# Optimization experiments

Measured on AMD Instinct MI355X. Metric: run time of the kernel, lower is better.

Reference implementation:

```python
import jax, jax.numpy as jnp
import numpy as np

N, E, IN_DIM, HID, OUT = 50000, 600000, 128, 256, 128

def setup_inputs() -> dict:
    key = jax.random.key(0)
    k1, k2, k3, k4, k5, k6, k7 = jax.random.split(key, 7)
    h = jax.random.normal(k1, (N, IN_DIM), dtype=jnp.float32)
    src = jax.random.randint(k2, (E,), 0, N)
    dst = jax.random.randint(k3, (E,), 0, N)
    s1 = 1.0 / np.sqrt(2 * IN_DIM)
    s2 = 1.0 / np.sqrt(HID)
    W1 = jax.random.uniform(k4, (2 * IN_DIM, HID), minval=-s1, maxval=s1, dtype=jnp.float32)
    b1 = jax.random.uniform(k5, (HID,), minval=-s1, maxval=s1, dtype=jnp.float32)
    W2 = jax.random.uniform(k6, (HID, OUT), minval=-s2, maxval=s2, dtype=jnp.float32)
    b2 = jax.random.uniform(k7, (OUT,), minval=-s2, maxval=s2, dtype=jnp.float32)
    return {"h": h, "src": src, "dst": dst, "W1": W1, "b1": b1, "W2": W2, "b2": b2}

def reference(h, src, dst, W1, b1, W2, b2):
    n = h.shape[0]
    # copy_u + mean: gather src features, segment-sum at dst, divide by in-degree
    msg_sum = jax.ops.segment_sum(h[src], dst, num_segments=n)          # [N, D]
    deg = jax.ops.segment_sum(jnp.ones((src.shape[0],), h.dtype), dst, num_segments=n)
    h_neigh = msg_sum / jnp.maximum(deg, 1.0)[:, None]                  # zero-deg nodes -> 0
    h_total = jnp.concatenate([h, h_neigh], axis=1)                     # [N, 2D]
    out = (h_total @ W1 + b1) @ W2 + b2                                 # 2-layer MLP (no inner activation)
    return jax.nn.relu(out)
```

## Files before the change

kernel.cpp:

```cpp
#include <hip/hip_runtime.h>

#define N_NODES 50000
#define E_EDGES 600000
#define IN_DIM  128
#define HID     256
#define OUT_DIM 128
#define CAP     64

#define NB_FILL 2344
#define NB_HCVT 6250
#define NB_WCVT 384
#define NB_PREP (NB_FILL + NB_HCVT + NB_WCVT)
#define NB_MLP  782

typedef __bf16 bf16x8 __attribute__((ext_vector_type(8)));
typedef float  f32x16 __attribute__((ext_vector_type(16)));
typedef unsigned short ushort8 __attribute__((ext_vector_type(8)));

__device__ __forceinline__ unsigned short f2bf(float f) {
    union { float f; unsigned int i; } v; v.f = f;
    unsigned int b = v.i;
    b += 0x7fffu + ((b >> 16) & 1u);
    return (unsigned short)(b >> 16);
}
__device__ __forceinline__ float bf2f(unsigned short u) {
    union { unsigned int i; float f; } v; v.i = ((unsigned int)u) << 16; return v.f;
}

__global__ void __launch_bounds__(256)
sage_prep(const int* __restrict__ src, const int* __restrict__ dst,
          int* __restrict__ counts, char* __restrict__ outb,
          const float* __restrict__ h, unsigned short* __restrict__ ht,
          const float* __restrict__ W1, const float* __restrict__ W2,
          unsigned short* __restrict__ w1sw, unsigned short* __restrict__ w2sw) {
    int i = blockIdx.x;
    int q = i >> 2, r = i & 3;
    int job, id;
    if (r == 1) { job = 0; id = q; }
    else {
        int oid = 3 * q + (r == 0 ? 0 : r - 1);
        if (oid < NB_HCVT)           { job = 1; id = oid; }
        else if (oid < NB_HCVT + NB_WCVT) { job = 2; id = oid - NB_HCVT; }
        else                         { job = 0; id = 2245 + (oid - (NB_HCVT + NB_WCVT)); }
    }

    if (job == 0) {
        int e = id * 256 + threadIdx.x;
        if (e < E_EDGES) {
            int d = dst[e];
            int slot = atomicAdd(counts + d, 1);
            if (slot < CAP)
                *((int*)(outb + (size_t)d * 512 + 256) + slot) = src[e];
        }
    } else if (job == 1) {
        int idx = id * 256 + threadIdx.x;
        if (idx < N_NODES * 32) {
            int n = idx >> 5, g = idx & 31;
            const float4 v = *(const float4*)(h + (size_t)n * IN_DIM + g * 4);
            ushort4 o;
            o.x = f2bf(v.x); o.y = f2bf(v.y); o.z = f2bf(v.z); o.w = f2bf(v.w);
            *(ushort4*)(ht + (size_t)n * 128 + g * 4) = o;
        }
    } else {
        int i1 = id * 256 + threadIdx.x;
        if (i1 < 65536) {
            int j = i1 & 7, n = (i1 >> 3) & 255, g = (i1 >> 11) & 1, ks = (i1 >> 12) & 3, c = i1 >> 14;
            int k = c * 64 + ks * 16 + g * 8 + j;
            w1sw[i1] = f2bf(W1[(size_t)k * HID + n]);
        } else {
            int i2 = i1 - 65536;
            int j = i2 & 7, n = (i2 >> 3) & 127, g = (i2 >> 10) & 1, ks = (i2 >> 11) & 7, c = (i2 >> 14) & 1;
            int k = c * 128 + ks * 16 + g * 8 + j;
            w2sw[i2] = f2bf(W2[(size_t)k * OUT_DIM + n]);
        }
    }
}

__global__ void __launch_bounds__(256)
sage_fused(const int* __restrict__ counts,
           const unsigned short* __restrict__ ht,
           const unsigned short* __restrict__ w1sw,
           const unsigned short* __restrict__ w2sw,
           const float* __restrict__ b1,
           const float* __restrict__ b2,
           float* out) {
    __shared__ unsigned short wbuf[16384];
    __shared__ unsigned short hid_s[64][264];

    const int t = threadIdx.x;
    const int nw = t >> 6;
    const int lane = t & 63;
    const int lr = lane & 31;
    const int lg = lane >> 5;
    const int base = blockIdx.x * 64;
    const int row0 = min(base + lr,      N_NODES - 1);
    const int row1 = min(base + 32 + lr, N_NODES - 1);

    {
        const bf16x8* gsrc = (const bf16x8*)(w1sw);
        #pragma unroll
        for (int i2 = 0; i2 < 8; ++i2) {
            int off16 = i2 * 256 + t;
            *(bf16x8*)(wbuf + off16 * 8) = gsrc[off16];
        }
    }

    {
        int node = base + (t >> 2);
        int l4 = t & 3;
        if (node < N_NODES) {
            int dg = counts[node];
            int entries = min(dg, CAP);
            const int* bk = (const int*)((const char*)out + (size_t)node * 512 + 256);
            float acc[32];
            #pragma unroll
            for (int j = 0; j < 32; ++j) acc[j] = 0.f;
            int e = 0;
            for (; e + 4 <= entries; e += 4) {
                const int4 sx = *(const int4*)(bk + e);
                const ushort8* p0 = (const ushort8*)(ht + (size_t)sx.x * 128 + l4 * 32);
                const ushort8* p1 = (const ushort8*)(ht + (size_t)sx.y * 128 + l4 * 32);
                const ushort8* p2 = (const ushort8*)(ht + (size_t)sx.z * 128 + l4 * 32);
                const ushort8* p3 = (const ushort8*)(ht + (size_t)sx.w * 128 + l4 * 32);
                ushort8 v00 = p0[0], v01 = p0[1], v02 = p0[2], v03 = p0[3];
                ushort8 v10 = p1[0], v11 = p1[1], v12 = p1[2], v13 = p1[3];
                ushort8 v20 = p2[0], v21 = p2[1], v22 = p2[2], v23 = p2[3];
                ushort8 v30 = p3[0], v31 = p3[1], v32 = p3[2], v33 = p3[3];
                #pragma unroll
                for (int j = 0; j < 8; ++j) {
                    acc[j]      += bf2f(v00[j]) + bf2f(v10[j]) + bf2f(v20[j]) + bf2f(v30[j]);
                    acc[8 + j]  += bf2f(v01[j]) + bf2f(v11[j]) + bf2f(v21[j]) + bf2f(v31[j]);
                    acc[16 + j] += bf2f(v02[j]) + bf2f(v12[j]) + bf2f(v22[j]) + bf2f(v32[j]);
                    acc[24 + j] += bf2f(v03[j]) + bf2f(v13[j]) + bf2f(v23[j]) + bf2f(v33[j]);
                }
            }
            for (; e < entries; ++e) {
                const ushort8* p = (const ushort8*)(ht + (size_t)bk[e] * 128 + l4 * 32);
                ushort8 w0 = p[0], w1v = p[1], w2v = p[2], w3 = p[3];
                #pragma unroll
                for (int j = 0; j < 8; ++j) {
                    acc[j]      += bf2f(w0[j]);
                    acc[8 + j]  += bf2f(w1v[j]);
                    acc[16 + j] += bf2f(w2v[j]);
                    acc[24 + j] += bf2f(w3[j]);
                }
            }
            float inv = 1.0f / (float)max(dg, 1);
            int m = t >> 2;
            #pragma unroll
            for (int qq = 0; qq < 4; ++qq) {
                ushort8 o;
                #pragma unroll
                for (int j = 0; j < 8; ++j) o[j] = f2bf(acc[qq * 8 + j] * inv);
                *(ushort8*)(&hid_s[m][l4 * 32 + qq * 8]) = o;
            }
        }
    }

    f32x16 c1[2][2];
    #pragma unroll
    for (int e2 = 0; e2 < 16; ++e2) {
        c1[0][0][e2] = 0.f; c1[0][1][e2] = 0.f; c1[1][0][e2] = 0.f; c1[1][1][e2] = 0.f;
    }

    #pragma unroll
    for (int c = 0; c < 4; ++c) {
        if (c) {
            __syncthreads();
            const bf16x8* gsrc = (const bf16x8*)(w1sw + c * 16384);
            #pragma unroll
            for (int i2 = 0; i2 < 8; ++i2) {
                int off16 = i2 * 256 + t;
                *(bf16x8*)(wbuf + off16 * 8) = gsrc[off16];
            }
        }
        bf16x8 a0[4], a1[4];
        #pragma unroll
        for (int ks = 0; ks < 4; ++ks) {
            if (c < 2) {
                int koff = (c * 4 + ks) * 16 + lg * 8;
                a0[ks] = *(const bf16x8*)(ht + (size_t)row0 * 128 + koff);
                a1[ks] = *(const bf16x8*)(ht + (size_t)row1 * 128 + koff);
            } else {
                int koff = (c - 2) * 64 + ks * 16 + lg * 8;
                a0[ks] = *(const bf16x8*)(&hid_s[lr][koff]);
                a1[ks] = *(const bf16x8*)(&hid_s[32 + lr][koff]);
            }
        }
        __syncthreads();
        #pragma unroll
        for (int ks = 0; ks < 4; ++ks) {
            #pragma unroll
            for (int nt = 0; nt < 2; ++nt) {
                int n = nw * 64 + nt * 32 + lr;
                bf16x8 b = *(const bf16x8*)(wbuf + (((ks * 2 + lg) * 256) + n) * 8);
                c1[0][nt] = __builtin_amdgcn_mfma_f32_32x32x16_bf16(a0[ks], b, c1[0][nt], 0, 0, 0);
                c1[1][nt] = __builtin_amdgcn_mfma_f32_32x32x16_bf16(a1[ks], b, c1[1][nt], 0, 0, 0);
            }
        }
    }

    #pragma unroll
    for (int nt = 0; nt < 2; ++nt) {
        int col = nw * 64 + nt * 32 + lr;
        float bias = b1[col];
        #pragma unroll
        for (int s = 0; s < 2; ++s) {
            #pragma unroll
            for (int reg = 0; reg < 16; ++reg) {
                int m = s * 32 + (reg & 3) + 8 * (reg >> 2) + 4 * lg;
                hid_s[m][col] = f2bf(c1[s][nt][reg] + bias);
            }
        }
    }
    __syncthreads();

    f32x16 c2[2];
    #pragma unroll
    for (int e2 = 0; e2 < 16; ++e2) { c2[0][e2] = 0.f; c2[1][e2] = 0.f; }

    #pragma unroll
    for (int c = 0; c < 2; ++c) {
        if (c) __syncthreads();
        {
            const bf16x8* gsrc = (const bf16x8*)(w2sw + c * 16384);
            #pragma unroll
            for (int i2 = 0; i2 < 8; ++i2) {
                int off16 = i2 * 256 + t;
                *(bf16x8*)(wbuf + off16 * 8) = gsrc[off16];
            }
        }
        __syncthreads();
        #pragma unroll
        for (int ks = 0; ks < 8; ++ks) {
            bf16x8 b = *(const bf16x8*)(wbuf + ((ks * 2 + lg) * 128 + nw * 32 + lr) * 8);
            int koff = c * 128 + ks * 16 + lg * 8;
            bf16x8 ah0 = *(const bf16x8*)(&hid_s[lr][koff]);
            bf16x8 ah1 = *(const bf16x8*)(&hid_s[32 + lr][koff]);
            c2[0] = __builtin_amdgcn_mfma_f32_32x32x16_bf16(ah0, b, c2[0], 0, 0, 0);
            c2[1] = __builtin_amdgcn_mfma_f32_32x32x16_bf16(ah1, b, c2[1], 0, 0, 0);
        }
    }

    {
        int col = nw * 32 + lr;
        float bias = b2[col];
        #pragma unroll
        for (int s = 0; s < 2; ++s) {
            #pragma unroll
            for (int reg = 0; reg < 16; ++reg) {
                int m = s * 32 + (reg & 3) + 8 * (reg >> 2) + 4 * lg;
                int n = base + m;
                if (n < N_NODES)
                    out[(size_t)n * OUT_DIM + col] = fmaxf(c2[s][reg] + bias, 0.0f);
            }
        }
    }
}

extern "C" void kernel_launch(void* const* d_in, const int* in_sizes, int n_in,
                              void* d_out, int out_size, void* d_ws, size_t ws_size,
                              hipStream_t stream) {
    const float* h   = (const float*)d_in[0];
    const int*   src = (const int*)d_in[1];
    const int*   dst = (const int*)d_in[2];
    const float* W1  = (const float*)d_in[3];
    const float* b1  = (const float*)d_in[4];
    const float* W2  = (const float*)d_in[5];
    const float* b2  = (const float*)d_in[6];
    float* out = (float*)d_out;

    int* counts = (int*)d_ws;
    unsigned short* w1sw = (unsigned short*)(counts + N_NODES);
    unsigned short* w2sw = w1sw + 65536;
    unsigned short* ht   = w2sw + 32768;

    hipMemsetAsync(counts, 0, N_NODES * sizeof(int), stream);

    sage_prep<<<NB_PREP, 256, 0, stream>>>(
        src, dst, counts, (char*)d_out, h, ht, W1, W2, w1sw, w2sw);

    sage_fused<<<NB_MLP, 256, 0, stream>>>(counts, ht, w1sw, w2sw, b1, b2, out);
}
```

Baseline: 183.9 us.

## Read MFMA weight fragments directly from global memory and vectorize prep kernel

Removes the LDS weight staging buffer in the fused kernel; B fragments for both GEMMs are now loaded straight from global/L2, which eliminates most __syncthreads and frees 32KB of LDS per block so more blocks can reside per CU (launch_bounds 256,4). The prep kernel is restructured into contiguous block ranges, with each thread handling four edges and eight features via vector loads. The gather loop prefetches the next group of four neighbor indices. The trade-off is more global/L2 traffic for weights (every wave rereads them) in exchange for higher occupancy and fewer barriers.

```diff
diff --git a/kernel.cpp b/kernel.cpp
--- a/kernel.cpp
+++ b/kernel.cpp
@@ -7,11 +7,11 @@
 #define OUT_DIM 128
 #define CAP     64
 
-#define NB_FILL 2344
-#define NB_HCVT 6250
-#define NB_WCVT 384
-#define NB_PREP (NB_FILL + NB_HCVT + NB_WCVT)
-#define NB_MLP  782
+#define NB_FILL4 586
+#define NB_HCVT8 3125
+#define NB_WCVT  384
+#define NB_PREP  (NB_FILL4 + NB_HCVT8 + NB_WCVT)
+#define NB_MLP   782
 
 typedef __bf16 bf16x8 __attribute__((ext_vector_type(8)));
 typedef float  f32x16 __attribute__((ext_vector_type(16)));
@@ -33,36 +33,33 @@
           const float* __restrict__ h, unsigned short* __restrict__ ht,
           const float* __restrict__ W1, const float* __restrict__ W2,
           unsigned short* __restrict__ w1sw, unsigned short* __restrict__ w2sw) {
-    int i = blockIdx.x;
-    int q = i >> 2, r = i & 3;
-    int job, id;
-    if (r == 1) { job = 0; id = q; }
-    else {
-        int oid = 3 * q + (r == 0 ? 0 : r - 1);
-        if (oid < NB_HCVT)           { job = 1; id = oid; }
-        else if (oid < NB_HCVT + NB_WCVT) { job = 2; id = oid - NB_HCVT; }
-        else                         { job = 0; id = 2245 + (oid - (NB_HCVT + NB_WCVT)); }
-    }
-
-    if (job == 0) {
-        int e = id * 256 + threadIdx.x;
-        if (e < E_EDGES) {
-            int d = dst[e];
-            int slot = atomicAdd(counts + d, 1);
-            if (slot < CAP)
-                *((int*)(outb + (size_t)d * 512 + 256) + slot) = src[e];
-        }
-    } else if (job == 1) {
-        int idx = id * 256 + threadIdx.x;
-        if (idx < N_NODES * 32) {
-            int n = idx >> 5, g = idx & 31;
-            const float4 v = *(const float4*)(h + (size_t)n * IN_DIM + g * 4);
-            ushort4 o;
-            o.x = f2bf(v.x); o.y = f2bf(v.y); o.z = f2bf(v.z); o.w = f2bf(v.w);
-            *(ushort4*)(ht + (size_t)n * 128 + g * 4) = o;
-        }
+    int b = blockIdx.x;
+    if (b < NB_FILL4) {
+        int e4 = (b * 256 + threadIdx.x) * 4;
+        if (e4 < E_EDGES) {
+            const int4 s4 = *(const int4*)(src + e4);
+            const int4 d4 = *(const int4*)(dst + e4);
+            int sl;
+            sl = atomicAdd(counts + d4.x, 1);
+            if (sl < CAP) *((int*)(outb + (size_t)d4.x * 512 + 256) + sl) = s4.x;
+            sl = atomicAdd(counts + d4.y, 1);
+            if (sl < CAP) *((int*)(outb + (size_t)d4.y * 512 + 256) + sl) = s4.y;
+            sl = atomicAdd(counts + d4.z, 1);
+            if (sl < CAP) *((int*)(outb + (size_t)d4.z * 512 + 256) + sl) = s4.z;
+            sl = atomicAdd(counts + d4.w, 1);
+            if (sl < CAP) *((int*)(outb + (size_t)d4.w * 512 + 256) + sl) = s4.w;
+        }
+    } else if (b < NB_FILL4 + NB_HCVT8) {
+        int idx = (b - NB_FILL4) * 256 + threadIdx.x;
+        int n = idx >> 4, g = idx & 15;
+        const float4 v0 = *(const float4*)(h + (size_t)n * IN_DIM + g * 8);
+        const float4 v1 = *(const float4*)(h + (size_t)n * IN_DIM + g * 8 + 4);
+        ushort8 o;
+        o[0] = f2bf(v0.x); o[1] = f2bf(v0.y); o[2] = f2bf(v0.z); o[3] = f2bf(v0.w);
+        o[4] = f2bf(v1.x); o[5] = f2bf(v1.y); o[6] = f2bf(v1.z); o[7] = f2bf(v1.w);
+        *(ushort8*)(ht + (size_t)n * 128 + g * 8) = o;
     } else {
-        int i1 = id * 256 + threadIdx.x;
+        int i1 = (b - NB_FILL4 - NB_HCVT8) * 256 + threadIdx.x;
         if (i1 < 65536) {
             int j = i1 & 7, n = (i1 >> 3) & 255, g = (i1 >> 11) & 1, ks = (i1 >> 12) & 3, c = i1 >> 14;
             int k = c * 64 + ks * 16 + g * 8 + j;
@@ -76,7 +73,7 @@
     }
 }
 
-__global__ void __launch_bounds__(256)
+__global__ void __launch_bounds__(256, 4)
 sage_fused(const int* __restrict__ counts,
            const unsigned short* __restrict__ ht,
            const unsigned short* __restrict__ w1sw,
@@ -84,7 +81,6 @@
            const float* __restrict__ b1,
            const float* __restrict__ b2,
            float* out) {
-    __shared__ unsigned short wbuf[16384];
     __shared__ unsigned short hid_s[64][264];
 
     const int t = threadIdx.x;
@@ -97,15 +93,6 @@
     const int row1 = min(base + 32 + lr, N_NODES - 1);
 
     {
-        const bf16x8* gsrc = (const bf16x8*)(w1sw);
-        #pragma unroll
-        for (int i2 = 0; i2 < 8; ++i2) {
-            int off16 = i2 * 256 + t;
-            *(bf16x8*)(wbuf + off16 * 8) = gsrc[off16];
-        }
-    }
-
-    {
         int node = base + (t >> 2);
         int l4 = t & 3;
         if (node < N_NODES) {
@@ -115,9 +102,10 @@
             float acc[32];
             #pragma unroll
             for (int j = 0; j < 32; ++j) acc[j] = 0.f;
+            int4 sx = *(const int4*)(bk);
             int e = 0;
             for (; e + 4 <= entries; e += 4) {
-                const int4 sx = *(const int4*)(bk + e);
+                const int4 nx = *(const int4*)(bk + min(e + 4, CAP - 4));
                 const ushort8* p0 = (const ushort8*)(ht + (size_t)sx.x * 128 + l4 * 32);
                 const ushort8* p1 = (const ushort8*)(ht + (size_t)sx.y * 128 + l4 * 32);
                 const ushort8* p2 = (const ushort8*)(ht + (size_t)sx.z * 128 + l4 * 32);
@@ -133,6 +121,7 @@
                     acc[16 + j] += bf2f(v02[j]) + bf2f(v12[j]) + bf2f(v22[j]) + bf2f(v32[j]);
                     acc[24 + j] += bf2f(v03[j]) + bf2f(v13[j]) + bf2f(v23[j]) + bf2f(v33[j]);
                 }
+                sx = nx;
             }
             for (; e < entries; ++e) {
                 const ushort8* p = (const ushort8*)(ht + (size_t)bk[e] * 128 + l4 * 32);
@@ -164,41 +153,50 @@
     }
 
     #pragma unroll
-    for (int c = 0; c < 4; ++c) {
-        if (c) {
-            __syncthreads();
-            const bf16x8* gsrc = (const bf16x8*)(w1sw + c * 16384);
-            #pragma unroll
-            for (int i2 = 0; i2 < 8; ++i2) {
-                int off16 = i2 * 256 + t;
-                *(bf16x8*)(wbuf + off16 * 8) = gsrc[off16];
-            }
-        }
+    for (int c = 0; c < 2; ++c) {
         bf16x8 a0[4], a1[4];
         #pragma unroll
         for (int ks = 0; ks < 4; ++ks) {
-            if (c < 2) {
-                int koff = (c * 4 + ks) * 16 + lg * 8;
-                a0[ks] = *(const bf16x8*)(ht + (size_t)row0 * 128 + koff);
-                a1[ks] = *(const bf16x8*)(ht + (size_t)row1 * 128 + koff);
-            } else {
-                int koff = (c - 2) * 64 + ks * 16 + lg * 8;
-                a0[ks] = *(const bf16x8*)(&hid_s[lr][koff]);
-                a1[ks] = *(const bf16x8*)(&hid_s[32 + lr][koff]);
-            }
-        }
-        __syncthreads();
+            int koff = (c * 4 + ks) * 16 + lg * 8;
+            a0[ks] = *(const bf16x8*)(ht + (size_t)row0 * 128 + koff);
+            a1[ks] = *(const bf16x8*)(ht + (size_t)row1 * 128 + koff);
+        }
         #pragma unroll
         for (int ks = 0; ks < 4; ++ks) {
             #pragma unroll
             for (int nt = 0; nt < 2; ++nt) {
                 int n = nw * 64 + nt * 32 + lr;
-                bf16x8 b = *(const bf16x8*)(wbuf + (((ks * 2 + lg) * 256) + n) * 8);
+                bf16x8 b = *(const bf16x8*)(w1sw + c * 16384 + (((ks * 2 + lg) * 256) + n) * 8);
                 c1[0][nt] = __builtin_amdgcn_mfma_f32_32x32x16_bf16(a0[ks], b, c1[0][nt], 0, 0, 0);
                 c1[1][nt] = __builtin_amdgcn_mfma_f32_32x32x16_bf16(a1[ks], b, c1[1][nt], 0, 0, 0);
             }
         }
     }
+
+    __syncthreads();
+
+    #pragma unroll
+    for (int c = 2; c < 4; ++c) {
+        bf16x8 a0[4], a1[4];
+        #pragma unroll
+        for (int ks = 0; ks < 4; ++ks) {
+            int koff = (c - 2) * 64 + ks * 16 + lg * 8;
+            a0[ks] = *(const bf16x8*)(&hid_s[lr][koff]);
+            a1[ks] = *(const bf16x8*)(&hid_s[32 + lr][koff]);
+        }
+        #pragma unroll
+        for (int ks = 0; ks < 4; ++ks) {
+            #pragma unroll
+            for (int nt = 0; nt < 2; ++nt) {
+                int n = nw * 64 + nt * 32 + lr;
+                bf16x8 b = *(const bf16x8*)(w1sw + c * 16384 + (((ks * 2 + lg) * 256) + n) * 8);
+                c1[0][nt] = __builtin_amdgcn_mfma_f32_32x32x16_bf16(a0[ks], b, c1[0][nt], 0, 0, 0);
+                c1[1][nt] = __builtin_amdgcn_mfma_f32_32x32x16_bf16(a1[ks], b, c1[1][nt], 0, 0, 0);
+            }
+        }
+    }
+
+    __syncthreads();
 
     #pragma unroll
     for (int nt = 0; nt < 2; ++nt) {
@@ -221,19 +219,9 @@
 
     #pragma unroll
     for (int c = 0; c < 2; ++c) {
-        if (c) __syncthreads();
-        {
-            const bf16x8* gsrc = (const bf16x8*)(w2sw + c * 16384);
-            #pragma unroll
-            for (int i2 = 0; i2 < 8; ++i2) {
-                int off16 = i2 * 256 + t;
-                *(bf16x8*)(wbuf + off16 * 8) = gsrc[off16];
-            }
-        }
-        __syncthreads();
         #pragma unroll
         for (int ks = 0; ks < 8; ++ks) {
-            bf16x8 b = *(const bf16x8*)(wbuf + ((ks * 2 + lg) * 128 + nw * 32 + lr) * 8);
+            bf16x8 b = *(const bf16x8*)(w2sw + c * 16384 + ((ks * 2 + lg) * 128 + nw * 32 + lr) * 8);
             int koff = c * 128 + ks * 16 + lg * 8;
             bf16x8 ah0 = *(const bf16x8*)(&hid_s[lr][koff]);
             bf16x8 ah1 = *(const bf16x8*)(&hid_s[32 + lr][koff]);
```

Measured after the change: 181.7 us. About the same (-1.2%).
